# Kernel optimization log

Measured on AMD Instinct MI355X. Metric: run time of the kernel, lower is better.

## Reference

```python
import jax, jax.numpy as jnp
import numpy as np

IN_DIM, HID, HEADS, OUT_DIM = 768, 128, 4, 256
SEM = HID * HEADS  # 512
N_USER, N_LLM, E = 50000, 5000, 400000


def gat_conv(x_src, x_dst, src, dst, W_src, W_dst, att_src, att_dst, bias, n_dst):
    """PyG GATConv (bipartite, concat=True), eval mode (no dropout)."""
    H, C = att_src.shape
    hs = (x_src @ W_src).reshape(-1, H, C)  # [Ns,H,C]
    hd = (x_dst @ W_dst).reshape(-1, H, C)  # [Nd,H,C]
    a_s = (hs * att_src).sum(-1)            # [Ns,H]
    a_d = (hd * att_dst).sum(-1)            # [Nd,H]
    e = jax.nn.leaky_relu(a_s[src] + a_d[dst], 0.2)  # [E,H]
    m = jax.ops.segment_max(e, dst, num_segments=n_dst)
    m = jnp.where(jnp.isfinite(m), m, 0.0)
    ex = jnp.exp(e - m[dst])
    denom = jax.ops.segment_sum(ex, dst, num_segments=n_dst)
    alpha = ex / (denom[dst] + 1e-16)        # [E,H]
    msg = hs[src] * alpha[:, :, None]        # [E,H,C]
    out = jax.ops.segment_sum(msg, dst, num_segments=n_dst)  # [Nd,H,C]
    return out.reshape(n_dst, H * C) + bias


def setup_inputs() -> dict:
    key = jax.random.key(0)
    ks = jax.random.split(key, 20)
    s = lambda k, shape, sc: jax.random.normal(k, shape, jnp.float32) * sc
    d = {
        'x_user': jax.random.normal(ks[0], (N_USER, IN_DIM), jnp.float32),
        'x_llm': jax.random.normal(ks[1], (N_LLM, IN_DIM), jnp.float32),
        'src0': jax.random.randint(ks[2], (E,), 0, N_LLM, jnp.int32),
        'dst0': jax.random.randint(ks[3], (E,), 0, N_USER, jnp.int32),
        'src1': jax.random.randint(ks[4], (E,), 0, N_USER, jnp.int32),
        'dst1': jax.random.randint(ks[5], (E,), 0, N_USER, jnp.int32),
    }
    sc_in = 1.0 / np.sqrt(IN_DIM)
    for i in range(2):
        d[f'Wsrc{i}'] = s(ks[6 + 5 * i], (IN_DIM, HEADS * HID), sc_in)
        d[f'Wdst{i}'] = s(ks[7 + 5 * i], (IN_DIM, HEADS * HID), sc_in)
        d[f'asrc{i}'] = s(ks[8 + 5 * i], (HEADS, HID), 1.0 / np.sqrt(HID))
        d[f'adst{i}'] = s(ks[9 + 5 * i], (HEADS, HID), 1.0 / np.sqrt(HID))
        d[f'bias{i}'] = jnp.zeros((HEADS * HID,), jnp.float32)
    d['sem_W1'] = s(ks[16], (SEM, 128), 1.0 / np.sqrt(SEM))
    d['sem_b1'] = jnp.zeros((128,), jnp.float32)
    d['sem_W2'] = s(ks[17], (128, 1), 1.0 / np.sqrt(128))
    d['out_W'] = s(ks[18], (SEM, OUT_DIM), 1.0 / np.sqrt(SEM))
    d['out_b'] = jnp.zeros((OUT_DIM,), jnp.float32)
    return d


def reference(x_user, x_llm, src0, dst0, src1, dst1,
              Wsrc0, Wdst0, asrc0, adst0, bias0,
              Wsrc1, Wdst1, asrc1, adst1, bias1,
              sem_W1, sem_b1, sem_W2, out_W, out_b):
    # metapath 0: llm -> user ; metapath 1: user -> user
    z0 = jax.nn.elu(gat_conv(x_llm, x_user, src0, dst0,
                             Wsrc0, Wdst0, asrc0, adst0, bias0, N_USER))
    z1 = jax.nn.elu(gat_conv(x_user, x_user, src1, dst1,
                             Wsrc1, Wdst1, asrc1, adst1, bias1, N_USER))
    z = jnp.stack([z0, z1], axis=1)  # [N, P=2, SEM]
    w = jnp.tanh(z @ sem_W1 + sem_b1) @ sem_W2  # [N,P,1]
    beta = jax.nn.softmax(w, axis=1)
    z_final = (beta * z).sum(axis=1)  # [N, SEM]
    return z_final @ out_W + out_b    # [N, OUT_DIM]
```

## Files before the change

### kernel.cpp

```cpp
#include <hip/hip_runtime.h>
#include <hip/hip_bf16.h>
#include <math.h>

constexpr int IN_DIM  = 768;
constexpr int HID     = 128;
constexpr int OUT_DIM = 256;
constexpr int SEM     = 512;
constexpr int N_USER  = 50000;
constexpr int N_LLM   = 5000;
constexpr int NE      = 400000;

constexpr int MP_USER = 50048;
constexpr int MP_LLM  = 5120;
constexpr int MP_2U   = 100096;
constexpr int GY_USER = MP_USER / 128;
constexpr int GY_LLM  = MP_LLM / 128;

typedef unsigned int uint;
typedef unsigned short ushort;
typedef __attribute__((ext_vector_type(8))) short bf16x8;
typedef __attribute__((ext_vector_type(4))) float f32x4;

constexpr int cdiv(int a, int b) { return (a + b - 1) / b; }

__device__ __forceinline__ ushort f2b(float f) {
  uint u = __float_as_uint(f);
  u += 0x7FFFu + ((u >> 16) & 1u);
  return (ushort)(u >> 16);
}
__device__ __forceinline__ float b2f(uint bits16) {
  return __uint_as_float(bits16 << 16);
}

__device__ __forceinline__ float fexp2(float x) { return __builtin_amdgcn_exp2f(x); }
#define LOG2E 1.4426950408889634f

#define GLOAD_LDS16(g, l) __builtin_amdgcn_global_load_lds( \
    (const __attribute__((address_space(1))) void*)(g), \
    (__attribute__((address_space(3))) void*)(l), 16, 0, 0)


__global__ __launch_bounds__(256) void gemm_bf16_0(
    const ushort* __restrict__ A, const ushort* __restrict__ Bt,
    ushort* __restrict__ Cout, int N, int K)
{
  __shared__ ushort As[128][64];
  __shared__ ushort Bs[128][64];
  const int t = threadIdx.x;
  const int wid = t >> 6, lane = t & 63;

  const int nwg  = gridDim.x * gridDim.y;
  const int orig = blockIdx.y * gridDim.x + blockIdx.x;
  const int q = nwg >> 3, r = nwg & 7;
  const int xcd = orig & 7, idx = orig >> 3;
  const int swz = (xcd < r ? xcd * (q + 1) : r * (q + 1) + (xcd - r) * q) + idx;
  const int bxi = swz % gridDim.x, byi = swz / gridDim.x;

  const int bm = byi * 128, bn = bxi * 128;
  const int lr = lane & 15, kg = lane >> 4;
  const int sw8 = lr & 7;
  const int mbase = (wid >> 1) * 64, nbase = (wid & 1) * 64;
  const int grow = lane >> 3;
  const int gcol = (((lane & 7) ^ grow)) * 8;

  f32x4 acc[4][4] = {};

  for (int k0 = 0; k0 < K; k0 += 64) {
#pragma unroll
    for (int c = 0; c < 4; ++c) {
      int ch = wid * 4 + c;
      GLOAD_LDS16(A  + (size_t)(bm + ch * 8 + grow) * K + k0 + gcol, &As[ch * 8][0]);
      GLOAD_LDS16(Bt + (size_t)(bn + ch * 8 + grow) * K + k0 + gcol, &Bs[ch * 8][0]);
    }
    asm volatile("s_waitcnt vmcnt(0)" ::: "memory");
    __syncthreads();
#pragma unroll
    for (int kb = 0; kb < 2; ++kb) {
      const int csw = ((kb * 4 + kg) ^ sw8) * 8;
      bf16x8 av[4], bv[4];
#pragma unroll
      for (int m = 0; m < 4; ++m)
        av[m] = *(const bf16x8*)&As[mbase + m * 16 + lr][csw];
#pragma unroll
      for (int n = 0; n < 4; ++n)
        bv[n] = *(const bf16x8*)&Bs[nbase + n * 16 + lr][csw];
#pragma unroll
      for (int m = 0; m < 4; ++m)
#pragma unroll
        for (int n = 0; n < 4; ++n)
          acc[m][n] = __builtin_amdgcn_mfma_f32_16x16x32_bf16(av[m], bv[n], acc[m][n], 0, 0, 0);
    }
    __syncthreads();
  }

#pragma unroll
  for (int m = 0; m < 4; ++m)
#pragma unroll
    for (int j = 0; j < 4; ++j) {
      int row = bm + mbase + m * 16 + kg * 4 + j;
#pragma unroll
      for (int n = 0; n < 4; ++n) {
        int col = bn + nbase + n * 16 + lr;
        Cout[(size_t)row * N + col] = f2b(acc[m][n][j]);
      }
    }
}

__global__ __launch_bounds__(256) void gemm_hs(
    const ushort* __restrict__ A_u, const ushort* __restrict__ A_l,
    const ushort* __restrict__ Bt_u, const ushort* __restrict__ Bt_l,
    ushort* __restrict__ hs_u, ushort* __restrict__ hs_l,
    float* __restrict__ logU, float* __restrict__ logL)
{
  __shared__ ushort As[128][64];
  __shared__ ushort Bs[128][64];
  const int t = threadIdx.x;
  const int wid = t >> 6, lane = t & 63;
  const int K = IN_DIM;

  const int nwg  = gridDim.x * gridDim.y;
  const int orig = blockIdx.y * gridDim.x + blockIdx.x;
  const int q = nwg >> 3, r = nwg & 7;
  const int xcd = orig & 7, idx = orig >> 3;
  const int swz = (xcd < r ? xcd * (q + 1) : r * (q + 1) + (xcd - r) * q) + idx;
  const int bxi = swz % gridDim.x, byi0 = swz / gridDim.x;

  const bool llm = (byi0 >= GY_USER);
  const int byi = llm ? byi0 - GY_USER : byi0;
  const ushort* A    = llm ? A_l : A_u;
  const ushort* Bt   = llm ? Bt_l : Bt_u;
  ushort* hs         = llm ? hs_l : hs_u;
  float* logit       = llm ? logL : logU;

  const int bm = byi * 128, bn = bxi * 128;
  const int lr = lane & 15, kg = lane >> 4;
  const int sw8 = lr & 7;
  const int mbase = (wid >> 1) * 64, nbase = (wid & 1) * 64;
  const int grow = lane >> 3;
  const int gcol = (((lane & 7) ^ grow)) * 8;

  f32x4 acc[4][4] = {};

  for (int k0 = 0; k0 < K; k0 += 64) {
#pragma unroll
    for (int c = 0; c < 4; ++c) {
      int ch = wid * 4 + c;
      GLOAD_LDS16(A  + (size_t)(bm + ch * 8 + grow) * K + k0 + gcol, &As[ch * 8][0]);
      GLOAD_LDS16(Bt + (size_t)(bn + ch * 8 + grow) * K + k0 + gcol, &Bs[ch * 8][0]);
    }
    asm volatile("s_waitcnt vmcnt(0)" ::: "memory");
    __syncthreads();
#pragma unroll
    for (int kb = 0; kb < 2; ++kb) {
      const int csw = ((kb * 4 + kg) ^ sw8) * 8;
      bf16x8 av[4], bv[4];
#pragma unroll
      for (int m = 0; m < 4; ++m)
        av[m] = *(const bf16x8*)&As[mbase + m * 16 + lr][csw];
#pragma unroll
      for (int n = 0; n < 4; ++n)
        bv[n] = *(const bf16x8*)&Bs[nbase + n * 16 + lr][csw];
#pragma unroll
      for (int m = 0; m < 4; ++m)
#pragma unroll
        for (int n = 0; n < 4; ++n)
          acc[m][n] = __builtin_amdgcn_mfma_f32_16x16x32_bf16(av[m], bv[n], acc[m][n], 0, 0, 0);
    }
    __syncthreads();
  }

  if (bxi == (int)gridDim.x - 1) {
    if (nbase == 0) {
#pragma unroll
      for (int m = 0; m < 4; ++m)
#pragma unroll
        for (int j = 0; j < 4; ++j) {
          int row = bm + mbase + m * 16 + kg * 4 + j;
          logit[(size_t)row * 16 + lr] = acc[m][0][j];
        }
    }
    return;
  }

#pragma unroll
  for (int m = 0; m < 4; ++m)
#pragma unroll
    for (int j = 0; j < 4; ++j) {
      int row = bm + mbase + m * 16 + kg * 4 + j;
#pragma unroll
      for (int n = 0; n < 4; ++n) {
        int col = bn + nbase + n * 16 + lr;
        hs[(size_t)row * SEM + col] = f2b(acc[m][n][j]);
      }
    }
}

__global__ __launch_bounds__(256) void gemm_out(
    const ushort* __restrict__ Z, const ushort* __restrict__ WtO,
    float* __restrict__ out, const float* __restrict__ out_b,
    const float2* __restrict__ beta)
{
  __shared__ ushort As[128][64];
  __shared__ ushort Bs[256][64];
  const int t = threadIdx.x;
  const int wid = t >> 6, lane = t & 63;
  const int K = SEM;

  const int nwg  = gridDim.x;
  const int orig = blockIdx.x;
  const int q = nwg >> 3, r = nwg & 7;
  const int xcd = orig & 7, idx = orig >> 3;
  const int swz = (xcd < r ? xcd * (q + 1) : r * (q + 1) + (xcd - r) * q) + idx;

  const int bm = swz * 128;
  const int lr = lane & 15, kg = lane >> 4;
  const int sw8 = lr & 7;
  const int mbase = (wid >> 1) * 64, nbase = (wid & 1) * 128;
  const int grow = lane >> 3;
  const int gcol = (((lane & 7) ^ grow)) * 8;
  const int wcol = (((lane & 7) ^ grow)) * 8;

  f32x4 acc[4][8] = {};

  for (int k0 = 0; k0 < K; k0 += 64) {
#pragma unroll
    for (int c = 0; c < 8; ++c) {
      int ch = wid * 8 + c;
      GLOAD_LDS16(WtO + (size_t)(ch * 8 + grow) * K + k0 + gcol, &Bs[ch * 8][0]);
    }
#pragma unroll
    for (int c = 0; c < 4; ++c) {
      int ch = wid * 4 + c;
      int rl = ch * 8 + grow;
      int row = bm + rl;
      const ushort* z0p = Z + (size_t)row * SEM + k0 + (lane & 7) * 8;
      const ushort* z1p = Z + (size_t)(N_USER + row) * SEM + k0 + (lane & 7) * 8;
      float2 bb = beta[row];
      uint4 a0 = *(const uint4*)z0p;
      uint4 a1 = *(const uint4*)z1p;
      uint rpk[4];
#pragma unroll
      for (int qq = 0; qq < 4; ++qq) {
        uint x0 = ((const uint*)&a0)[qq], x1 = ((const uint*)&a1)[qq];
        float lo = bb.x * b2f(x0 & 0xffffu) + bb.y * b2f(x1 & 0xffffu);
        float hi = bb.x * b2f(x0 >> 16)     + bb.y * b2f(x1 >> 16);
        rpk[qq] = (uint)f2b(lo) | ((uint)f2b(hi) << 16);
      }
      *(uint4*)&As[rl][wcol] = make_uint4(rpk[0], rpk[1], rpk[2], rpk[3]);
    }
    asm volatile("s_waitcnt vmcnt(0)" ::: "memory");
    __syncthreads();
#pragma unroll
    for (int kb = 0; kb < 2; ++kb) {
      const int csw = ((kb * 4 + kg) ^ sw8) * 8;
      bf16x8 av[4], bv[8];
#pragma unroll
      for (int m = 0; m < 4; ++m)
        av[m] = *(const bf16x8*)&As[mbase + m * 16 + lr][csw];
#pragma unroll
      for (int n = 0; n < 8; ++n)
        bv[n] = *(const bf16x8*)&Bs[nbase + n * 16 + lr][csw];
#pragma unroll
      for (int m = 0; m < 4; ++m)
#pragma unroll
        for (int n = 0; n < 8; ++n)
          acc[m][n] = __builtin_amdgcn_mfma_f32_16x16x32_bf16(av[m], bv[n], acc[m][n], 0, 0, 0);
    }
    __syncthreads();
  }

#pragma unroll
  for (int m = 0; m < 4; ++m)
#pragma unroll
    for (int j = 0; j < 4; ++j) {
      int row = bm + mbase + m * 16 + kg * 4 + j;
      if (row >= N_USER) continue;
#pragma unroll
      for (int n = 0; n < 8; ++n) {
        int col = nbase + n * 16 + lr;
        out[(size_t)row * OUT_DIM + col] = acc[m][n][j] + out_b[col];
      }
    }
}

constexpr int NB_FOLD  = cdiv(IN_DIM * 16, 256);
constexpr int NB_CASTU = N_USER * IN_DIM / 8 / 256;
constexpr int NB_CASTL = N_LLM * IN_DIM / 8 / 256;
constexpr int NB_TTW   = (IN_DIM / 64) * (SEM / 64);
constexpr int NB_TTS   = (SEM / 64) * (HID / 64);
constexpr int NB_TTO   = (SEM / 64) * (OUT_DIM / 64);
constexpr int NB_E1    = cdiv(2 * NE, 256);
constexpr int PB0 = NB_FOLD;
constexpr int PB1 = PB0 + NB_CASTU;
constexpr int PB2 = PB1 + NB_CASTL;
constexpr int PB3 = PB2 + NB_TTW;
constexpr int PB4 = PB3 + NB_TTW;
constexpr int PB5 = PB4 + NB_TTS;
constexpr int PB6 = PB5 + NB_TTO;
constexpr int PB7 = PB6 + NB_E1;
constexpr int PREP_GRID = 2048;

__device__ __forceinline__ void tt_body(const float* __restrict__ W,
                                        ushort* __restrict__ Bt,
                                        int K, int Nw, int tile,
                                        float (*lds)[65], int t)
{
  const int tiles_n = Nw >> 6;
  const int tk = tile / tiles_n, tn = tile - tk * tiles_n;
  const int k0 = tk << 6, n0 = tn << 6;
#pragma unroll
  for (int i = 0; i < 16; ++i) {
    int idx = t + i * 256;
    int rr = idx >> 6, cc = idx & 63;
    lds[rr][cc] = W[(size_t)(k0 + rr) * Nw + n0 + cc];
  }
  __syncthreads();
#pragma unroll
  for (int i = 0; i < 4; ++i) {
    int idx = t + i * 256;
    int cc = idx >> 4;
    int rq = (idx & 15) * 4;
    uint lo = (uint)f2b(lds[rq][cc])     | ((uint)f2b(lds[rq + 1][cc]) << 16);
    uint hi = (uint)f2b(lds[rq + 2][cc]) | ((uint)f2b(lds[rq + 3][cc]) << 16);
    *(uint2*)(Bt + (size_t)(n0 + cc) * K + k0 + rq) = make_uint2(lo, hi);
  }
  __syncthreads();
}

__device__ __forceinline__ void cast_body(const float* __restrict__ x,
                                          ushort* __restrict__ xb, int i)
{
  const float4 a = *(const float4*)(x + (size_t)i * 8);
  const float4 c = *(const float4*)(x + (size_t)i * 8 + 4);
  uint4 o;
  o.x = (uint)f2b(a.x) | ((uint)f2b(a.y) << 16);
  o.y = (uint)f2b(a.z) | ((uint)f2b(a.w) << 16);
  o.z = (uint)f2b(c.x) | ((uint)f2b(c.y) << 16);
  o.w = (uint)f2b(c.z) | ((uint)f2b(c.w) << 16);
  *(uint4*)(xb + (size_t)i * 8) = o;
}

__global__ __launch_bounds__(256) void prep_kernel(
    const float* __restrict__ x_user, const float* __restrict__ x_llm,
    ushort* __restrict__ xb_u, ushort* __restrict__ xb_l,
    const float* __restrict__ Wdst0, const float* __restrict__ adst0,
    const float* __restrict__ Wdst1, const float* __restrict__ adst1,
    const float* __restrict__ Wsrc1, const float* __restrict__ asrc1,
    const float* __restrict__ Wsrc0, const float* __restrict__ asrc0,
    ushort* __restrict__ Wt1x, ushort* __restrict__ Wt0x,
    const float* __restrict__ sem_W1, ushort* __restrict__ WtS,
    const float* __restrict__ out_W, ushort* __restrict__ WtO,
    const int* __restrict__ dst0, const int* __restrict__ dst1,
    int* __restrict__ deg, int* __restrict__ rank)
{
  __shared__ float lds[64][65];
  const int t = threadIdx.x;
  for (int b = blockIdx.x; b < PB7; b += PREP_GRID) {
    if (b < PB0) {
      int idxg = b * 256 + t;
      if (idxg < IN_DIM * 16) {
        int k = idxg >> 4, hh = idxg & 15;
        const float* W;
        const float* att;
        if (hh < 4)       { W = Wdst0; att = adst0; }
        else if (hh < 8)  { W = Wdst1; att = adst1; }
        else if (hh < 12) { W = Wsrc1; att = asrc1; }
        else              { W = Wsrc0; att = asrc0; }
        int h = hh & 3;
        float s = 0.f;
#pragma unroll 4
        for (int c = 0; c < HID; ++c)
          s += W[(size_t)k * SEM + h * HID + c] * att[h * HID + c];
        if (hh < 12) Wt1x[(size_t)(512 + hh) * IN_DIM + k] = f2b(s);
        else         Wt0x[(size_t)(512 + h) * IN_DIM + k] = f2b(s);
      }
    } else if (b < PB1) {
      cast_body(x_user, xb_u, (b - PB0) * 256 + t);
    } else if (b < PB2) {
      cast_body(x_llm, xb_l, (b - PB1) * 256 + t);
    } else if (b < PB3) {
      tt_body(Wsrc0, Wt0x, IN_DIM, SEM, b - PB2, lds, t);
    } else if (b < PB4) {
      tt_body(Wsrc1, Wt1x, IN_DIM, SEM, b - PB3, lds, t);
    } else if (b < PB5) {
      tt_body(sem_W1, WtS, SEM, HID, b - PB4, lds, t);
    } else if (b < PB6) {
      tt_body(out_W, WtO, SEM, OUT_DIM, b - PB5, lds, t);
    } else {
      int e = (b - PB6) * 256 + t;
      if (e < 2 * NE) {
        int d = (e < NE) ? dst0[e] : (dst1[e - NE] + N_USER);
        rank[e] = atomicAdd(&deg[d], 1);
      }
    }
  }
}

__global__ void scatter_kernel(const int* __restrict__ src0, const int* __restrict__ dst0,
                               const int* __restrict__ src1, const int* __restrict__ dst1,
                               const int* __restrict__ rp, const int* __restrict__ rank,
                               ushort* __restrict__ scsr)
{
  for (int e = blockIdx.x * 256 + threadIdx.x; e < 2 * NE; e += gridDim.x * 256) {
    bool p1 = (e >= NE);
    int ee = p1 ? e - NE : e;
    int s = p1 ? src1[ee] : src0[ee];
    int d = p1 ? (dst1[ee] + N_USER) : dst0[ee];
    scsr[rp[d] + rank[e]] = (ushort)s;
  }
}

__global__ __launch_bounds__(256) void scan1(const int* __restrict__ deg,
                                             int* __restrict__ bsum, int n)
{
  __shared__ int sm[256];
  int b = blockIdx.x, t = threadIdx.x;
  int base = b * 1024 + t * 4;
  int s = 0;
#pragma unroll
  for (int i = 0; i < 4; ++i) if (base + i < n) s += deg[base + i];
  sm[t] = s;
  __syncthreads();
  for (int off = 128; off > 0; off >>= 1) {
    if (t < off) sm[t] += sm[t + off];
    __syncthreads();
  }
  if (t == 0) bsum[b] = sm[0];
}

__global__ __launch_bounds__(128) void scan2(const int* __restrict__ bsum,
                                             int* __restrict__ boff, int nb,
                                             int* __restrict__ rp_tail, int tailval)
{
  __shared__ int sm[128];
  int t = threadIdx.x;
  int v = (t < nb) ? bsum[t] : 0;
  sm[t] = v;
  __syncthreads();
  for (int off = 1; off < 128; off <<= 1) {
    int x = (t >= off) ? sm[t - off] : 0;
    __syncthreads();
    sm[t] += x;
    __syncthreads();
  }
  if (t < nb) boff[t] = sm[t] - v;
  if (t == 0) *rp_tail = tailval;
}

__global__ __launch_bounds__(256) void scan3(const int* __restrict__ deg,
                                             const int* __restrict__ boff,
                                             int* __restrict__ rp, int n)
{
  __shared__ int sm[256];
  int b = blockIdx.x, t = threadIdx.x;
  int base = b * 1024 + t * 4;
  int v[4];
#pragma unroll
  for (int i = 0; i < 4; ++i) v[i] = (base + i < n) ? deg[base + i] : 0;
  int tsum = v[0] + v[1] + v[2] + v[3];
  sm[t] = tsum;
  __syncthreads();
  for (int off = 1; off < 256; off <<= 1) {
    int x = (t >= off) ? sm[t - off] : 0;
    __syncthreads();
    sm[t] += x;
    __syncthreads();
  }
  int run = sm[t] - tsum + boff[b];
#pragma unroll
  for (int i = 0; i < 4; ++i) {
    if (base + i < n) rp[base + i] = run;
    run += v[i];
  }
}

__global__ __launch_bounds__(64) void agg_kernel(
    const ushort* __restrict__ hs0, const ushort* __restrict__ hs1,
    const ushort* __restrict__ srcs,
    const float* __restrict__ logitL, const float* __restrict__ logitU,
    const int* __restrict__ rp,
    const float* __restrict__ bias0, const float* __restrict__ bias1,
    ushort* __restrict__ Zout)
{
  __shared__ ushort s_src[64];
  __shared__ float  s_ev[64][4];
  int node = blockIdx.x, lane = threadIdx.x;
  bool p1 = (node >= N_USER);
  const ushort* hs   = p1 ? hs1 : hs0;
  const float*  bias = p1 ? bias1 : bias0;
  int nd = p1 ? node - N_USER : node;
  float4 ad4 = *(const float4*)(logitU + (size_t)nd * 16 + (p1 ? 4 : 0));
  ad4.x *= LOG2E; ad4.y *= LOG2E; ad4.z *= LOG2E; ad4.w *= LOG2E;
  const float* asbase = p1 ? (logitU + 8) : logitL;
  int h  = lane >> 4;
  int cb = lane * 8;
  float acc[8] = {};
  float dsum = 0.f;
  int jb = rp[node], je = rp[node + 1];
  for (int j0 = jb; j0 < je; j0 += 64) {
    int n = min(64, je - j0);
    __syncthreads();
    if (lane < n) {
      int s = srcs[j0 + lane];
      s_src[lane] = (ushort)s;
      float4 as4 = *(const float4*)(asbase + (size_t)s * 16);
      float v0 = as4.x * LOG2E + ad4.x, v1 = as4.y * LOG2E + ad4.y;
      float v2 = as4.z * LOG2E + ad4.z, v3 = as4.w * LOG2E + ad4.w;
      v0 = (v0 > 0.f) ? v0 : 0.2f * v0;
      v1 = (v1 > 0.f) ? v1 : 0.2f * v1;
      v2 = (v2 > 0.f) ? v2 : 0.2f * v2;
      v3 = (v3 > 0.f) ? v3 : 0.2f * v3;
      s_ev[lane][0] = fexp2(v0);
      s_ev[lane][1] = fexp2(v1);
      s_ev[lane][2] = fexp2(v2);
      s_ev[lane][3] = fexp2(v3);
    }
    __syncthreads();
#pragma unroll 4
    for (int j = 0; j < n; ++j) {
      int s = __builtin_amdgcn_readfirstlane((int)s_src[j]);
      float e = s_ev[j][h];
      const uint4 pv = *(const uint4*)(hs + ((size_t)s << 9) + cb);
      acc[0] += b2f(pv.x & 0xffffu) * e;  acc[1] += b2f(pv.x >> 16) * e;
      acc[2] += b2f(pv.y & 0xffffu) * e;  acc[3] += b2f(pv.y >> 16) * e;
      acc[4] += b2f(pv.z & 0xffffu) * e;  acc[5] += b2f(pv.z >> 16) * e;
      acc[6] += b2f(pv.w & 0xffffu) * e;  acc[7] += b2f(pv.w >> 16) * e;
      dsum += e;
    }
  }
  float inv = 1.f / (dsum + 1e-16f);
  float4 b4a = *(const float4*)(bias + cb);
  float4 b4b = *(const float4*)(bias + cb + 4);
  float bb[8] = { b4a.x, b4a.y, b4a.z, b4a.w, b4b.x, b4b.y, b4b.z, b4b.w };
  uint4 o;
  uint* op = (uint*)&o;
#pragma unroll
  for (int i = 0; i < 4; ++i) {
    float z0 = acc[2 * i]     * inv + bb[2 * i];
    float z1 = acc[2 * i + 1] * inv + bb[2 * i + 1];
    z0 = (z0 > 0.f) ? z0 : fexp2(z0 * LOG2E) - 1.f;
    z1 = (z1 > 0.f) ? z1 : fexp2(z1 * LOG2E) - 1.f;
    op[i] = (uint)f2b(z0) | ((uint)f2b(z1) << 16);
  }
  *(uint4*)(Zout + (size_t)node * SEM + cb) = o;
}

__global__ __launch_bounds__(256) void beta_kernel(
    const ushort* __restrict__ T, const float* __restrict__ b1,
    const float* __restrict__ W2, float2* __restrict__ beta, int n)
{
  int wid = threadIdx.x >> 6, lane = threadIdx.x & 63;
  int node = blockIdx.x * 4 + wid;
  if (node >= n) return;
  const ushort* t0 = T + (size_t)node * HID;
  const ushort* t1 = T + (size_t)(N_USER + node) * HID;
  int j = 2 * lane;
  uint u0 = *(const uint*)(t0 + j);
  uint u1 = *(const uint*)(t1 + j);
  float wa = W2[j], wb = W2[j + 1];
  float ba = b1[j], bb = b1[j + 1];
  auto ftanh = [](float x) {
    x = fminf(fmaxf(x, -20.f), 20.f);
    float e = fexp2(2.f * LOG2E * x);
    return (e - 1.f) / (e + 1.f);
  };
  float s0 = ftanh(b2f(u0 & 0xffffu) + ba) * wa + ftanh(b2f(u0 >> 16) + bb) * wb;
  float s1 = ftanh(b2f(u1 & 0xffffu) + ba) * wa + ftanh(b2f(u1 >> 16) + bb) * wb;
#pragma unroll
  for (int off = 32; off > 0; off >>= 1) {
    s0 += __shfl_down(s0, off);
    s1 += __shfl_down(s1, off);
  }
  if (lane == 0) {
    float mx = fmaxf(s0, s1);
    float e0 = fexp2((s0 - mx) * LOG2E), e1 = fexp2((s1 - mx) * LOG2E);
    float s = e0 + e1;
    beta[node] = make_float2(e0 / s, e1 / s);
  }
}

extern "C" void kernel_launch(void* const* d_in, const int* in_sizes, int n_in,
                              void* d_out, int out_size, void* d_ws, size_t ws_size,
                              hipStream_t stream)
{
  const float* x_user = (const float*)d_in[0];
  const float* x_llm  = (const float*)d_in[1];
  const int* src0 = (const int*)d_in[2];
  const int* dst0 = (const int*)d_in[3];
  const int* src1 = (const int*)d_in[4];
  const int* dst1 = (const int*)d_in[5];
  const float* Wsrc0 = (const float*)d_in[6];
  const float* Wdst0 = (const float*)d_in[7];
  const float* asrc0 = (const float*)d_in[8];
  const float* adst0 = (const float*)d_in[9];
  const float* bias0 = (const float*)d_in[10];
  const float* Wsrc1 = (const float*)d_in[11];
  const float* Wdst1 = (const float*)d_in[12];
  const float* asrc1 = (const float*)d_in[13];
  const float* adst1 = (const float*)d_in[14];
  const float* bias1 = (const float*)d_in[15];
  const float* sem_W1 = (const float*)d_in[16];
  const float* sem_b1 = (const float*)d_in[17];
  const float* sem_W2 = (const float*)d_in[18];
  const float* out_W  = (const float*)d_in[19];
  const float* out_b  = (const float*)d_in[20];

  char* ws = (char*)d_ws;
  size_t off = 0;
  auto alloc = [&](size_t bytes) -> size_t {
    size_t o = off;
    off += (bytes + 255) & ~(size_t)255;
    return o;
  };

  size_t xbu_off  = alloc((size_t)MP_USER * IN_DIM * 2);
  size_t xbl_off  = alloc((size_t)MP_LLM  * IN_DIM * 2);
  size_t wt0_off  = alloc((size_t)640 * IN_DIM * 2);
  size_t wt1_off  = alloc((size_t)640 * IN_DIM * 2);
  size_t wts_off  = alloc((size_t)HID * SEM * 2);
  size_t wto_off  = alloc((size_t)OUT_DIM * SEM * 2);
  size_t hs0_off  = alloc((size_t)MP_LLM  * SEM * 2);
  size_t hs1_off  = alloc((size_t)MP_USER * SEM * 2);
  size_t Z_off    = alloc((size_t)MP_2U   * SEM * 2);
  size_t sc_off   = alloc((size_t)2 * NE * 2);
  size_t rank_off = alloc((size_t)2 * NE * 4);
  size_t lgu_off  = alloc((size_t)MP_USER * 16 * 4);
  size_t lgl_off  = alloc((size_t)MP_LLM  * 16 * 4);
  size_t beta_off = alloc((size_t)MP_USER * 8);
  size_t deg_off  = alloc((size_t)2 * N_USER * 4);
  size_t zero_end = off;
  size_t rp_off   = alloc((size_t)(2 * N_USER + 1) * 4);
  size_t bs_off   = alloc((size_t)128 * 4);
  size_t bo_off   = alloc((size_t)128 * 4);

  ushort* xb_u  = (ushort*)(ws + xbu_off);
  ushort* xb_l  = (ushort*)(ws + xbl_off);
  ushort* Wt0x  = (ushort*)(ws + wt0_off);
  ushort* Wt1x  = (ushort*)(ws + wt1_off);
  ushort* WtS   = (ushort*)(ws + wts_off);
  ushort* WtO   = (ushort*)(ws + wto_off);
  ushort* hs0b  = (ushort*)(ws + hs0_off);
  ushort* hs1b  = (ushort*)(ws + hs1_off);
  ushort* Zsw   = (ushort*)(ws + Z_off);
  ushort* Tbuf  = (ushort*)(ws + xbu_off);
  ushort* scsr  = (ushort*)(ws + sc_off);
  int*    rank  = (int*)(ws + rank_off);
  float*  logU  = (float*)(ws + lgu_off);
  float*  logL  = (float*)(ws + lgl_off);
  float2* beta  = (float2*)(ws + beta_off);
  int*    deg   = (int*)(ws + deg_off);
  int*    rp    = (int*)(ws + rp_off);
  int*    bsum  = (int*)(ws + bs_off);
  int*    boff  = (int*)(ws + bo_off);

  hipMemsetAsync(ws + deg_off, 0, zero_end - deg_off, stream);
  hipMemsetAsync(Wt0x + (size_t)512 * IN_DIM, 0, (size_t)128 * IN_DIM * 2, stream);
  hipMemsetAsync(Wt1x + (size_t)512 * IN_DIM, 0, (size_t)128 * IN_DIM * 2, stream);

  prep_kernel<<<PREP_GRID, 256, 0, stream>>>(
      x_user, x_llm, xb_u, xb_l,
      Wdst0, adst0, Wdst1, adst1, Wsrc1, asrc1, Wsrc0, asrc0,
      Wt1x, Wt0x, sem_W1, WtS, out_W, WtO,
      dst0, dst1, deg, rank);

  const int NTOT = 2 * N_USER;
  const int NB = cdiv(NTOT, 1024);
  scan1<<<NB, 256, 0, stream>>>(deg, bsum, NTOT);
  scan2<<<1, 128, 0, stream>>>(bsum, boff, NB, rp + NTOT, 2 * NE);
  scan3<<<NB, 256, 0, stream>>>(deg, boff, rp, NTOT);
  scatter_kernel<<<2048, 256, 0, stream>>>(src0, dst0, src1, dst1, rp, rank, scsr);

  {
    dim3 g(640 / 128, GY_USER + GY_LLM);
    gemm_hs<<<g, 256, 0, stream>>>(xb_u, xb_l, Wt1x, Wt0x, hs1b, hs0b, logU, logL);
  }

  agg_kernel<<<NTOT, 64, 0, stream>>>(hs0b, hs1b, scsr, logL, logU, rp,
                                      bias0, bias1, Zsw);

  {
    dim3 g(HID / 128, MP_2U / 128);
    gemm_bf16_0<<<g, 256, 0, stream>>>(Zsw, WtS, Tbuf, HID, SEM);
  }

  beta_kernel<<<cdiv(N_USER, 4), 256, 0, stream>>>(Tbuf, sem_b1, sem_W2, beta, N_USER);

  gemm_out<<<GY_USER, 256, 0, stream>>>(Zsw, WtO, (float*)d_out, out_b, beta);
}
```

Measured before the change: 382.5 us.

## Widen hs GEMM tiles to 128x256 and interleave metapath rows in Z

```diff
diff --git a/kernel.cpp b/kernel.cpp
--- a/kernel.cpp
+++ b/kernel.cpp
@@ -40,6 +40,7 @@
     (__attribute__((address_space(3))) void*)(l), 16, 0, 0)
 
 
+
 __global__ __launch_bounds__(256) void gemm_bf16_0(
     const ushort* __restrict__ A, const ushort* __restrict__ Bt,
     ushort* __restrict__ Cout, int N, int K)
@@ -113,7 +114,7 @@
     float* __restrict__ logU, float* __restrict__ logL)
 {
   __shared__ ushort As[128][64];
-  __shared__ ushort Bs[128][64];
+  __shared__ ushort Bs[256][64];
   const int t = threadIdx.x;
   const int wid = t >> 6, lane = t & 63;
   const int K = IN_DIM;
@@ -132,44 +133,70 @@
   ushort* hs         = llm ? hs_l : hs_u;
   float* logit       = llm ? logL : logU;
 
-  const int bm = byi * 128, bn = bxi * 128;
+  const bool logt = (bxi == 2);
+  const int bm = byi * 128;
+  const int bnrow = logt ? 512 : bxi * 256;
   const int lr = lane & 15, kg = lane >> 4;
   const int sw8 = lr & 7;
-  const int mbase = (wid >> 1) * 64, nbase = (wid & 1) * 64;
+  const int mbase = (wid >> 1) * 64;
+  const int nbase = (wid & 1) * (logt ? 64 : 128);
   const int grow = lane >> 3;
   const int gcol = (((lane & 7) ^ grow)) * 8;
 
-  f32x4 acc[4][4] = {};
+  f32x4 acc[4][8] = {};
 
   for (int k0 = 0; k0 < K; k0 += 64) {
 #pragma unroll
     for (int c = 0; c < 4; ++c) {
       int ch = wid * 4 + c;
-      GLOAD_LDS16(A  + (size_t)(bm + ch * 8 + grow) * K + k0 + gcol, &As[ch * 8][0]);
-      GLOAD_LDS16(Bt + (size_t)(bn + ch * 8 + grow) * K + k0 + gcol, &Bs[ch * 8][0]);
+      GLOAD_LDS16(A + (size_t)(bm + ch * 8 + grow) * K + k0 + gcol, &As[ch * 8][0]);
+    }
+    if (logt) {
+#pragma unroll
+      for (int c = 0; c < 4; ++c) {
+        int ch = wid * 4 + c;
+        GLOAD_LDS16(Bt + (size_t)(bnrow + ch * 8 + grow) * K + k0 + gcol, &Bs[ch * 8][0]);
+      }
+    } else {
+#pragma unroll
+      for (int c = 0; c < 8; ++c) {
+        int ch = wid * 8 + c;
+        GLOAD_LDS16(Bt + (size_t)(bnrow + ch * 8 + grow) * K + k0 + gcol, &Bs[ch * 8][0]);
+      }
     }
     asm volatile("s_waitcnt vmcnt(0)" ::: "memory");
     __syncthreads();
 #pragma unroll
     for (int kb = 0; kb < 2; ++kb) {
       const int csw = ((kb * 4 + kg) ^ sw8) * 8;
-      bf16x8 av[4], bv[4];
+      bf16x8 av[4], bv[8];
 #pragma unroll
       for (int m = 0; m < 4; ++m)
         av[m] = *(const bf16x8*)&As[mbase + m * 16 + lr][csw];
-#pragma unroll
-      for (int n = 0; n < 4; ++n)
-        bv[n] = *(const bf16x8*)&Bs[nbase + n * 16 + lr][csw];
-#pragma unroll
-      for (int m = 0; m < 4; ++m)
+      if (logt) {
 #pragma unroll
         for (int n = 0; n < 4; ++n)
-          acc[m][n] = __builtin_amdgcn_mfma_f32_16x16x32_bf16(av[m], bv[n], acc[m][n], 0, 0, 0);
-    }
-    __syncthreads();
-  }
-
-  if (bxi == (int)gridDim.x - 1) {
+          bv[n] = *(const bf16x8*)&Bs[nbase + n * 16 + lr][csw];
+#pragma unroll
+        for (int m = 0; m < 4; ++m)
+#pragma unroll
+          for (int n = 0; n < 4; ++n)
+            acc[m][n] = __builtin_amdgcn_mfma_f32_16x16x32_bf16(av[m], bv[n], acc[m][n], 0, 0, 0);
+      } else {
+#pragma unroll
+        for (int n = 0; n < 8; ++n)
+          bv[n] = *(const bf16x8*)&Bs[nbase + n * 16 + lr][csw];
+#pragma unroll
+        for (int m = 0; m < 4; ++m)
+#pragma unroll
+          for (int n = 0; n < 8; ++n)
+            acc[m][n] = __builtin_amdgcn_mfma_f32_16x16x32_bf16(av[m], bv[n], acc[m][n], 0, 0, 0);
+      }
+    }
+    __syncthreads();
+  }
+
+  if (logt) {
     if (nbase == 0) {
 #pragma unroll
       for (int m = 0; m < 4; ++m)
@@ -188,8 +215,8 @@
     for (int j = 0; j < 4; ++j) {
       int row = bm + mbase + m * 16 + kg * 4 + j;
 #pragma unroll
-      for (int n = 0; n < 4; ++n) {
-        int col = bn + nbase + n * 16 + lr;
+      for (int n = 0; n < 8; ++n) {
+        int col = bxi * 256 + nbase + n * 16 + lr;
         hs[(size_t)row * SEM + col] = f2b(acc[m][n][j]);
       }
     }
@@ -233,8 +260,8 @@
       int ch = wid * 4 + c;
       int rl = ch * 8 + grow;
       int row = bm + rl;
-      const ushort* z0p = Z + (size_t)row * SEM + k0 + (lane & 7) * 8;
-      const ushort* z1p = Z + (size_t)(N_USER + row) * SEM + k0 + (lane & 7) * 8;
+      const ushort* z0p = Z + (size_t)(2 * row) * SEM + k0 + (lane & 7) * 8;
+      const ushort* z1p = z0p + SEM;
       float2 bb = beta[row];
       uint4 a0 = *(const uint4*)z0p;
       uint4 a1 = *(const uint4*)z1p;
@@ -542,7 +569,8 @@
     z1 = (z1 > 0.f) ? z1 : fexp2(z1 * LOG2E) - 1.f;
     op[i] = (uint)f2b(z0) | ((uint)f2b(z1) << 16);
   }
-  *(uint4*)(Zout + (size_t)node * SEM + cb) = o;
+  int zrow = 2 * nd + (p1 ? 1 : 0);
+  *(uint4*)(Zout + (size_t)zrow * SEM + cb) = o;
 }
 
 __global__ __launch_bounds__(256) void beta_kernel(
@@ -552,8 +580,8 @@
   int wid = threadIdx.x >> 6, lane = threadIdx.x & 63;
   int node = blockIdx.x * 4 + wid;
   if (node >= n) return;
-  const ushort* t0 = T + (size_t)node * HID;
-  const ushort* t1 = T + (size_t)(N_USER + node) * HID;
+  const ushort* t0 = T + (size_t)(2 * node) * HID;
+  const ushort* t1 = t0 + HID;
   int j = 2 * lane;
   uint u0 = *(const uint*)(t0 + j);
   uint u1 = *(const uint*)(t1 + j);
@@ -671,7 +699,7 @@
   scatter_kernel<<<2048, 256, 0, stream>>>(src0, dst0, src1, dst1, rp, rank, scsr);
 
   {
-    dim3 g(640 / 128, GY_USER + GY_LLM);
+    dim3 g(3, GY_USER + GY_LLM);
     gemm_hs<<<g, 256, 0, stream>>>(xb_u, xb_l, Wt1x, Wt0x, hs1b, hs0b, logU, logL);
   }
 
```

New measurement: 414.6 us. 1.08x slower.
